# Optimization experiments

Measured on AMD Instinct MI355X. Metric: run time of the kernel, lower is better.

The kernel has to match this reference:

```python
import jax, jax.numpy as jnp
import numpy as np


def setup_inputs() -> dict:
    key = jax.random.key(0)
    ks = jax.random.split(key, 7)
    B, T, D, H, L, NS = 8192, 64, 64, 256, 64, 64  # batch, time, state, hidden, latent, n_shifts
    K = D + L  # Koopman state dim = 128
    x = jax.random.normal(ks[0], (B, T, D), dtype=jnp.float32)
    # Encoder weights stored as [in, out] (math-equivalent to torch Linear).
    W0 = jax.random.normal(ks[1], (D, H), dtype=jnp.float32) / np.float32(np.sqrt(D))
    b0 = jnp.zeros((H,), dtype=jnp.float32)
    W1 = jax.random.normal(ks[2], (H, H), dtype=jnp.float32) / np.float32(np.sqrt(H))
    b1 = jnp.zeros((H,), dtype=jnp.float32)
    W2 = jax.random.normal(ks[3], (H, L), dtype=jnp.float32) / np.float32(np.sqrt(H))  # last layer: no bias
    # Koopman operator scaled so spectral norm ~< 1 (stable 63-step rollout).
    ko_W = jax.random.normal(ks[4], (K, K), dtype=jnp.float32) * np.float32(0.04)
    return {"x": x, "W0": W0, "b0": b0, "W1": W1, "b1": b1, "W2": W2,
            "ko_W": ko_W, "n_shifts": NS}


def reference(x, W0, b0, W1, b1, W2, ko_W, n_shifts):
    x = x[:, :n_shifts, :]                       # [B, NS, D]
    h = jax.nn.relu(x @ W0 + b0)                 # [B, NS, H]
    h = jax.nn.relu(h @ W1 + b1)                 # [B, NS, H]
    z = h @ W2                                   # [B, NS, L] (last layer: no ReLU, no bias)
    enc_gt = jnp.concatenate([x, z], axis=-1)    # [B, NS, D+L]
    z0 = enc_gt[:, 0, :]                         # [B, K]
    def step(c, _):
        nc = c @ ko_W                            # repeated application of ko
        return nc, nc
    _, traj = jax.lax.scan(step, z0, None, length=n_shifts - 1)  # [NS-1, B, K]
    enc_traj = jnp.concatenate([z0[:, None, :], jnp.moveaxis(traj, 0, 1)], axis=1)  # [B, NS, K]
    return enc_gt, enc_traj
```

## Files before the change

kernel.cpp:

```cpp
#include <hip/hip_runtime.h>


typedef __attribute__((ext_vector_type(8))) short short8;
typedef __attribute__((ext_vector_type(4))) float floatx4;

#define DEV __device__ __forceinline__

DEV short f2bf(float f) {
  unsigned u = __builtin_bit_cast(unsigned, f);
  unsigned r = u + 0x7fffu + ((u >> 16) & 1u);
  return (short)(r >> 16);
}

DEV floatx4 zero4() { return (floatx4){0.f, 0.f, 0.f, 0.f}; }

constexpr long ROWS     = 524288;
constexpr long GT_ELEMS = 67108864;
constexpr int  HS_STRIDE = 264;

__global__ void prep_kernel(const float* __restrict__ W0, const float* __restrict__ W1,
                            const float* __restrict__ W2, const float* __restrict__ koW,
                            float* __restrict__ Ppow, short* __restrict__ Wf0,
                            short* __restrict__ Wf1, short* __restrict__ Wf2) {
  int g = blockIdx.x * 256 + threadIdx.x;
  if (g < 2048) {
    int lane = g & 63; int ntkt = g >> 6;
    int n  = ((ntkt >> 1) << 4) + (lane & 15);
    int k0 = (ntkt & 1) * 32 + (lane >> 4) * 8;
    short8 v;
    #pragma unroll
    for (int j = 0; j < 8; ++j) v[j] = f2bf(W0[(k0 + j) * 256 + n]);
    *(short8*)(Wf0 + g * 8) = v;
  } else if (g < 10240) {
    int h = g - 2048;
    int lane = h & 63; int ntkt = h >> 6;
    int n  = ((ntkt >> 3) << 4) + (lane & 15);
    int k0 = (ntkt & 7) * 32 + (lane >> 4) * 8;
    short8 v;
    #pragma unroll
    for (int j = 0; j < 8; ++j) v[j] = f2bf(W1[(k0 + j) * 256 + n]);
    *(short8*)(Wf1 + h * 8) = v;
  } else if (g < 12288) {
    int h = g - 10240;
    int lane = h & 63; int ntkt = h >> 6;
    int n  = ((ntkt >> 3) << 4) + (lane & 15);
    int k0 = (ntkt & 7) * 32 + (lane >> 4) * 8;
    short8 v;
    #pragma unroll
    for (int j = 0; j < 8; ++j) v[j] = f2bf(W2[(k0 + j) * 64 + n]);
    *(short8*)(Wf2 + h * 8) = v;
  } else if (g < 12288 + 8192) {
    int h = g - 12288;
    if (h < 4096) {
      int e = h * 4; int row = e >> 7; int c = e & 127;
      float4 v;
      v.x = (c     == row) ? 1.f : 0.f;
      v.y = (c + 1 == row) ? 1.f : 0.f;
      v.z = (c + 2 == row) ? 1.f : 0.f;
      v.w = (c + 3 == row) ? 1.f : 0.f;
      ((float4*)Ppow)[h] = v;
    } else {
      ((float4*)(Ppow + 16384))[h - 4096] = ((const float4*)koW)[h - 4096];
    }
  }
}

__global__ __launch_bounds__(256) void pow_step(float* Ppow, int base) {
  __shared__ float Bs[128 * 128];
  const int tid = threadIdx.x;
  const int j  = (blockIdx.x >> 2) + 1;
  const int qt = blockIdx.x & 3;
  const float* Bm = Ppow + (long)base * 16384;
  #pragma unroll
  for (int i = 0; i < 16; ++i) {
    int f4 = tid + 256 * i;
    ((float4*)Bs)[f4] = ((const float4*)Bm)[f4];
  }
  __syncthreads();
  const int row = qt * 32 + (tid >> 3);
  const int cg  = (tid & 7) * 16;
  const float* Arow = Ppow + (long)j * 16384 + row * 128;
  float acc[16];
  #pragma unroll
  for (int c = 0; c < 16; ++c) acc[c] = 0.f;
  for (int kk = 0; kk < 128; kk += 4) {
    float4 a4 = *(const float4*)(Arow + kk);
    #pragma unroll
    for (int u = 0; u < 4; ++u) {
      float a = (u == 0) ? a4.x : (u == 1) ? a4.y : (u == 2) ? a4.z : a4.w;
      const float* brow = Bs + (kk + u) * 128 + cg;
      #pragma unroll
      for (int c = 0; c < 16; ++c) acc[c] = fmaf(a, brow[c], acc[c]);
    }
  }
  float* Out = Ppow + (long)(base + j) * 16384 + row * 128 + cg;
  #pragma unroll
  for (int c4 = 0; c4 < 4; ++c4) {
    float4 o; o.x = acc[c4*4]; o.y = acc[c4*4+1]; o.z = acc[c4*4+2]; o.w = acc[c4*4+3];
    *(float4*)(Out + c4 * 4) = o;
  }
}

__global__ void convP_kernel(const float* __restrict__ Ppow, short* __restrict__ Pf) {
  int g = blockIdx.x * 256 + threadIdx.x;
  int lane = g & 63;
  int kt   = (g >> 6) & 3;
  int nt   = g >> 8;
  int n  = nt * 16 + (lane & 15);
  int t  = n >> 7, c = n & 127;
  int k0 = kt * 32 + (lane >> 4) * 8;
  short8 v;
  #pragma unroll
  for (int j = 0; j < 8; ++j) v[j] = f2bf(Ppow[(long)t * 16384 + (k0 + j) * 128 + c]);
  *(short8*)(Pf + (long)g * 8) = v;
}

__global__ __launch_bounds__(256) void mlp_kernel(const float* __restrict__ x,
    const short* __restrict__ Wf0, const float* __restrict__ b0,
    const short* __restrict__ Wf1, const float* __restrict__ b1,
    const short* __restrict__ Wf2, float* __restrict__ out) {
  __shared__ short Hs[64 * HS_STRIDE];
  const int tid  = threadIdx.x;
  const int lane = tid & 63;
  const int wave = tid >> 6;
  const int l15  = lane & 15;
  const int q    = lane >> 4;
  const long rowBase = (long)blockIdx.x * 64;

  #pragma unroll
  for (int i = 0; i < 4; ++i) {
    int f4 = tid + 256 * i;
    int r = f4 >> 4, c4 = f4 & 15;
    float4 v = ((const float4*)(x + (rowBase + r) * 64))[c4];
    ((float4*)(out + (rowBase + r) * 128))[c4] = v;
  }

  floatx4 acc[16];
  #pragma unroll
  for (int nt = 0; nt < 16; ++nt) acc[nt] = zero4();

  #pragma unroll
  for (int kt = 0; kt < 2; ++kt) {
    const float* ap = x + (rowBase + wave * 16 + l15) * 64 + kt * 32 + q * 8;
    float4 a0 = ((const float4*)ap)[0];
    float4 a1 = ((const float4*)ap)[1];
    short8 af;
    af[0]=f2bf(a0.x); af[1]=f2bf(a0.y); af[2]=f2bf(a0.z); af[3]=f2bf(a0.w);
    af[4]=f2bf(a1.x); af[5]=f2bf(a1.y); af[6]=f2bf(a1.z); af[7]=f2bf(a1.w);
    #pragma unroll
    for (int nt = 0; nt < 16; ++nt) {
      short8 bf = *(const short8*)(Wf0 + ((nt * 2 + kt) * 64 + lane) * 8);
      acc[nt] = __builtin_amdgcn_mfma_f32_16x16x32_bf16(af, bf, acc[nt], 0, 0, 0);
    }
  }
  #pragma unroll
  for (int nt = 0; nt < 16; ++nt) {
    int col = nt * 16 + l15;
    float bias = b0[col];
    #pragma unroll
    for (int r = 0; r < 4; ++r) {
      float v = acc[nt][r] + bias;
      Hs[(wave * 16 + q * 4 + r) * HS_STRIDE + col] = f2bf(v > 0.f ? v : 0.f);
    }
    acc[nt] = zero4();
  }
  __syncthreads();

  #pragma unroll
  for (int kt = 0; kt < 8; ++kt) {
    short8 af = *(const short8*)(Hs + (wave * 16 + l15) * HS_STRIDE + kt * 32 + q * 8);
    #pragma unroll
    for (int nt = 0; nt < 16; ++nt) {
      short8 bf = *(const short8*)(Wf1 + ((nt * 8 + kt) * 64 + lane) * 8);
      acc[nt] = __builtin_amdgcn_mfma_f32_16x16x32_bf16(af, bf, acc[nt], 0, 0, 0);
    }
  }
  __syncthreads();
  #pragma unroll
  for (int nt = 0; nt < 16; ++nt) {
    int col = nt * 16 + l15;
    float bias = b1[col];
    #pragma unroll
    for (int r = 0; r < 4; ++r) {
      float v = acc[nt][r] + bias;
      Hs[(wave * 16 + q * 4 + r) * HS_STRIDE + col] = f2bf(v > 0.f ? v : 0.f);
    }
  }
  __syncthreads();

  floatx4 acc2[4];
  #pragma unroll
  for (int nt = 0; nt < 4; ++nt) acc2[nt] = zero4();
  #pragma unroll
  for (int kt = 0; kt < 8; ++kt) {
    short8 af = *(const short8*)(Hs + (wave * 16 + l15) * HS_STRIDE + kt * 32 + q * 8);
    #pragma unroll
    for (int nt = 0; nt < 4; ++nt) {
      short8 bf = *(const short8*)(Wf2 + ((nt * 8 + kt) * 64 + lane) * 8);
      acc2[nt] = __builtin_amdgcn_mfma_f32_16x16x32_bf16(af, bf, acc2[nt], 0, 0, 0);
    }
  }
  #pragma unroll
  for (int nt = 0; nt < 4; ++nt) {
    int col = nt * 16 + l15;
    #pragma unroll
    for (int r = 0; r < 4; ++r)
      out[(rowBase + wave * 16 + q * 4 + r) * 128 + 64 + col] = acc2[nt][r];
  }
}

__global__ __launch_bounds__(256) void traj_kernel(const float* __restrict__ enc_gt,
    const short* __restrict__ Pf, float* __restrict__ out) {
  const int tid  = threadIdx.x;
  const int lane = tid & 63;
  const int wave = tid >> 6;
  const int l15  = lane & 15;
  const int q    = lane >> 4;
  const int bb = blockIdx.x >> 5;
  const int nb = blockIdx.x & 31;
  const long rowBase = (long)bb * 64 + wave * 16;
  const int ntBase = nb * 16;

  floatx4 acc[16];
  #pragma unroll
  for (int nt = 0; nt < 16; ++nt) acc[nt] = zero4();

  #pragma unroll
  for (int kt = 0; kt < 4; ++kt) {
    const float* ap = enc_gt + (rowBase + l15) * 8192 + kt * 32 + q * 8;
    float4 a0 = ((const float4*)ap)[0];
    float4 a1 = ((const float4*)ap)[1];
    short8 af;
    af[0]=f2bf(a0.x); af[1]=f2bf(a0.y); af[2]=f2bf(a0.z); af[3]=f2bf(a0.w);
    af[4]=f2bf(a1.x); af[5]=f2bf(a1.y); af[6]=f2bf(a1.z); af[7]=f2bf(a1.w);
    #pragma unroll
    for (int nt = 0; nt < 16; ++nt) {
      short8 bf = *(const short8*)(Pf + (((long)(ntBase + nt) * 4 + kt) * 64 + lane) * 8);
      acc[nt] = __builtin_amdgcn_mfma_f32_16x16x32_bf16(af, bf, acc[nt], 0, 0, 0);
    }
  }
  #pragma unroll
  for (int nt = 0; nt < 16; ++nt) {
    long col = (long)(ntBase + nt) * 16 + l15;
    #pragma unroll
    for (int r = 0; r < 4; ++r)
      out[GT_ELEMS + (rowBase + q * 4 + r) * 8192 + col] = acc[nt][r];
  }
}

extern "C" void kernel_launch(void* const* d_in, const int* in_sizes, int n_in,
                              void* d_out, int out_size, void* d_ws, size_t ws_size,
                              hipStream_t stream) {
  (void)in_sizes; (void)n_in; (void)out_size; (void)ws_size;
  const float* x   = (const float*)d_in[0];
  const float* W0  = (const float*)d_in[1];
  const float* b0  = (const float*)d_in[2];
  const float* W1  = (const float*)d_in[3];
  const float* b1  = (const float*)d_in[4];
  const float* W2  = (const float*)d_in[5];
  const float* koW = (const float*)d_in[6];
  float* out = (float*)d_out;

  char* ws = (char*)d_ws;
  float* Ppow = (float*)ws;
  short* Pf   = (short*)(ws + 4194304);
  short* Wf0  = (short*)(ws + 6291456);
  short* Wf1  = (short*)(ws + 6324224);
  short* Wf2  = (short*)(ws + 6455296);

  hipLaunchKernelGGL(prep_kernel, dim3(80), dim3(256), 0, stream,
                     W0, W1, W2, koW, Ppow, Wf0, Wf1, Wf2);
  const int bases[6] = {1, 2, 4, 8, 16, 32};
  const int cnts[6]  = {1, 2, 4, 8, 16, 31};
  for (int s = 0; s < 6; ++s)
    hipLaunchKernelGGL(pow_step, dim3(cnts[s] * 4), dim3(256), 0, stream, Ppow, bases[s]);
  hipLaunchKernelGGL(convP_kernel, dim3(512), dim3(256), 0, stream, Ppow, Pf);
  hipLaunchKernelGGL(mlp_kernel, dim3(8192), dim3(256), 0, stream,
                     x, Wf0, b0, Wf1, b1, Wf2, out);
  hipLaunchKernelGGL(traj_kernel, dim3(4096), dim3(256), 0, stream, out, Pf, out);
}
```

Before: 1.120 ms.

## Split MFMA tiles across waves by N and stage A-tile in LDS

In both the MLP and trajectory kernels, each wave now owns a 4-column-tile slice of the output for all 64 rows, where before it owned 16 rows across every column tile. Each wave therefore loads only 4 B fragments per k-step instead of 16, which cuts redundant global weight and Pf reads across waves. The trajectory kernel also converts the block's 64x128 enc_gt tile to bf16 once into shared memory, replacing per-wave global loads and conversions. Launch bounds add a minimum of 4 blocks per CU, which caps register use and may cause spills. The kernel is dominated by the large trajectory output write, so the gain may be limited.

```diff
diff --git a/kernel.cpp b/kernel.cpp
--- a/kernel.cpp
+++ b/kernel.cpp
@@ -2,6 +2,7 @@
 
 
 typedef __attribute__((ext_vector_type(8))) short short8;
+typedef __attribute__((ext_vector_type(4))) short sshort4;
 typedef __attribute__((ext_vector_type(4))) float floatx4;
 
 #define DEV __device__ __forceinline__
@@ -17,6 +18,7 @@
 constexpr long ROWS     = 524288;
 constexpr long GT_ELEMS = 67108864;
 constexpr int  HS_STRIDE = 264;
+constexpr int  AS_STRIDE = 136;
 
 __global__ void prep_kernel(const float* __restrict__ W0, const float* __restrict__ W1,
                             const float* __restrict__ W2, const float* __restrict__ koW,
@@ -115,7 +117,7 @@
   *(short8*)(Pf + (long)g * 8) = v;
 }
 
-__global__ __launch_bounds__(256) void mlp_kernel(const float* __restrict__ x,
+__global__ __launch_bounds__(256, 4) void mlp_kernel(const float* __restrict__ x,
     const short* __restrict__ Wf0, const float* __restrict__ b0,
     const short* __restrict__ Wf1, const float* __restrict__ b1,
     const short* __restrict__ Wf2, float* __restrict__ out) {
@@ -125,6 +127,7 @@
   const int wave = tid >> 6;
   const int l15  = lane & 15;
   const int q    = lane >> 4;
+  const int ntg  = wave * 4;
   const long rowBase = (long)blockIdx.x * 64;
 
   #pragma unroll
@@ -135,82 +138,100 @@
     ((float4*)(out + (rowBase + r) * 128))[c4] = v;
   }
 
-  floatx4 acc[16];
-  #pragma unroll
-  for (int nt = 0; nt < 16; ++nt) acc[nt] = zero4();
+  floatx4 acc[4][4];
+  #pragma unroll
+  for (int m = 0; m < 4; ++m)
+    #pragma unroll
+    for (int nt = 0; nt < 4; ++nt) acc[m][nt] = zero4();
 
   #pragma unroll
   for (int kt = 0; kt < 2; ++kt) {
-    const float* ap = x + (rowBase + wave * 16 + l15) * 64 + kt * 32 + q * 8;
-    float4 a0 = ((const float4*)ap)[0];
-    float4 a1 = ((const float4*)ap)[1];
-    short8 af;
-    af[0]=f2bf(a0.x); af[1]=f2bf(a0.y); af[2]=f2bf(a0.z); af[3]=f2bf(a0.w);
-    af[4]=f2bf(a1.x); af[5]=f2bf(a1.y); af[6]=f2bf(a1.z); af[7]=f2bf(a1.w);
-    #pragma unroll
-    for (int nt = 0; nt < 16; ++nt) {
-      short8 bf = *(const short8*)(Wf0 + ((nt * 2 + kt) * 64 + lane) * 8);
-      acc[nt] = __builtin_amdgcn_mfma_f32_16x16x32_bf16(af, bf, acc[nt], 0, 0, 0);
-    }
-  }
-  #pragma unroll
-  for (int nt = 0; nt < 16; ++nt) {
-    int col = nt * 16 + l15;
+    short8 bfr[4];
+    #pragma unroll
+    for (int nt = 0; nt < 4; ++nt)
+      bfr[nt] = *(const short8*)(Wf0 + (((ntg + nt) * 2 + kt) * 64 + lane) * 8);
+    #pragma unroll
+    for (int m = 0; m < 4; ++m) {
+      const float* ap = x + (rowBase + m * 16 + l15) * 64 + kt * 32 + q * 8;
+      float4 a0 = ((const float4*)ap)[0];
+      float4 a1 = ((const float4*)ap)[1];
+      short8 af;
+      af[0]=f2bf(a0.x); af[1]=f2bf(a0.y); af[2]=f2bf(a0.z); af[3]=f2bf(a0.w);
+      af[4]=f2bf(a1.x); af[5]=f2bf(a1.y); af[6]=f2bf(a1.z); af[7]=f2bf(a1.w);
+      #pragma unroll
+      for (int nt = 0; nt < 4; ++nt)
+        acc[m][nt] = __builtin_amdgcn_mfma_f32_16x16x32_bf16(af, bfr[nt], acc[m][nt], 0, 0, 0);
+    }
+  }
+  #pragma unroll
+  for (int nt = 0; nt < 4; ++nt) {
+    int col = (ntg + nt) * 16 + l15;
     float bias = b0[col];
     #pragma unroll
-    for (int r = 0; r < 4; ++r) {
-      float v = acc[nt][r] + bias;
-      Hs[(wave * 16 + q * 4 + r) * HS_STRIDE + col] = f2bf(v > 0.f ? v : 0.f);
-    }
-    acc[nt] = zero4();
+    for (int m = 0; m < 4; ++m) {
+      #pragma unroll
+      for (int r = 0; r < 4; ++r) {
+        float v = acc[m][nt][r] + bias;
+        Hs[(m * 16 + q * 4 + r) * HS_STRIDE + col] = f2bf(v > 0.f ? v : 0.f);
+      }
+      acc[m][nt] = zero4();
+    }
   }
   __syncthreads();
 
   #pragma unroll
   for (int kt = 0; kt < 8; ++kt) {
-    short8 af = *(const short8*)(Hs + (wave * 16 + l15) * HS_STRIDE + kt * 32 + q * 8);
-    #pragma unroll
-    for (int nt = 0; nt < 16; ++nt) {
-      short8 bf = *(const short8*)(Wf1 + ((nt * 8 + kt) * 64 + lane) * 8);
-      acc[nt] = __builtin_amdgcn_mfma_f32_16x16x32_bf16(af, bf, acc[nt], 0, 0, 0);
-    }
-  }
-  __syncthreads();
-  #pragma unroll
-  for (int nt = 0; nt < 16; ++nt) {
-    int col = nt * 16 + l15;
+    short8 bfr[4];
+    #pragma unroll
+    for (int nt = 0; nt < 4; ++nt)
+      bfr[nt] = *(const short8*)(Wf1 + (((ntg + nt) * 8 + kt) * 64 + lane) * 8);
+    #pragma unroll
+    for (int m = 0; m < 4; ++m) {
+      short8 af = *(const short8*)(Hs + (m * 16 + l15) * HS_STRIDE + kt * 32 + q * 8);
+      #pragma unroll
+      for (int nt = 0; nt < 4; ++nt)
+        acc[m][nt] = __builtin_amdgcn_mfma_f32_16x16x32_bf16(af, bfr[nt], acc[m][nt], 0, 0, 0);
+    }
+  }
+  __syncthreads();
+  #pragma unroll
+  for (int nt = 0; nt < 4; ++nt) {
+    int col = (ntg + nt) * 16 + l15;
     float bias = b1[col];
     #pragma unroll
-    for (int r = 0; r < 4; ++r) {
-      float v = acc[nt][r] + bias;
-      Hs[(wave * 16 + q * 4 + r) * HS_STRIDE + col] = f2bf(v > 0.f ? v : 0.f);
+    for (int m = 0; m < 4; ++m) {
+      #pragma unroll
+      for (int r = 0; r < 4; ++r) {
+        float v = acc[m][nt][r] + bias;
+        Hs[(m * 16 + q * 4 + r) * HS_STRIDE + col] = f2bf(v > 0.f ? v : 0.f);
+      }
     }
   }
   __syncthreads();
 
   floatx4 acc2[4];
   #pragma unroll
-  for (int nt = 0; nt < 4; ++nt) acc2[nt] = zero4();
+  for (int m = 0; m < 4; ++m) acc2[m] = zero4();
   #pragma unroll
   for (int kt = 0; kt < 8; ++kt) {
-    short8 af = *(const short8*)(Hs + (wave * 16 + l15) * HS_STRIDE + kt * 32 + q * 8);
-    #pragma unroll
-    for (int nt = 0; nt < 4; ++nt) {
-      short8 bf = *(const short8*)(Wf2 + ((nt * 8 + kt) * 64 + lane) * 8);
-      acc2[nt] = __builtin_amdgcn_mfma_f32_16x16x32_bf16(af, bf, acc2[nt], 0, 0, 0);
-    }
-  }
-  #pragma unroll
-  for (int nt = 0; nt < 4; ++nt) {
-    int col = nt * 16 + l15;
+    short8 bfr = *(const short8*)(Wf2 + ((wave * 8 + kt) * 64 + lane) * 8);
+    #pragma unroll
+    for (int m = 0; m < 4; ++m) {
+      short8 af = *(const short8*)(Hs + (m * 16 + l15) * HS_STRIDE + kt * 32 + q * 8);
+      acc2[m] = __builtin_amdgcn_mfma_f32_16x16x32_bf16(af, bfr, acc2[m], 0, 0, 0);
+    }
+  }
+  #pragma unroll
+  for (int m = 0; m < 4; ++m) {
     #pragma unroll
     for (int r = 0; r < 4; ++r)
-      out[(rowBase + wave * 16 + q * 4 + r) * 128 + 64 + col] = acc2[nt][r];
-  }
-}
-
-__global__ __launch_bounds__(256) void traj_kernel(const float* __restrict__ enc_gt,
+      out[(rowBase + m * 16 + q * 4 + r) * 128 + 64 + wave * 16 + l15] = acc2[m][r];
+  }
+}
+
+__global__ __launch_bounds__(256, 4) void traj_kernel(const float* __restrict__ enc_gt,
     const short* __restrict__ Pf, float* __restrict__ out) {
+  __shared__ short As[64 * AS_STRIDE];
   const int tid  = threadIdx.x;
   const int lane = tid & 63;
   const int wave = tid >> 6;
@@ -218,33 +239,49 @@
   const int q    = lane >> 4;
   const int bb = blockIdx.x >> 5;
   const int nb = blockIdx.x & 31;
-  const long rowBase = (long)bb * 64 + wave * 16;
-  const int ntBase = nb * 16;
-
-  floatx4 acc[16];
-  #pragma unroll
-  for (int nt = 0; nt < 16; ++nt) acc[nt] = zero4();
+  const long rowBase = (long)bb * 64;
+  const int ntg = nb * 16 + wave * 4;
+
+  #pragma unroll
+  for (int i = 0; i < 8; ++i) {
+    int idx = tid + 256 * i;
+    int r = idx >> 5, c4 = idx & 31;
+    float4 v = ((const float4*)(enc_gt + (rowBase + r) * 8192))[c4];
+    sshort4 s;
+    s[0] = f2bf(v.x); s[1] = f2bf(v.y); s[2] = f2bf(v.z); s[3] = f2bf(v.w);
+    *(sshort4*)(As + r * AS_STRIDE + c4 * 4) = s;
+  }
+  __syncthreads();
+
+  floatx4 acc[4][4];
+  #pragma unroll
+  for (int m = 0; m < 4; ++m)
+    #pragma unroll
+    for (int nt = 0; nt < 4; ++nt) acc[m][nt] = zero4();
 
   #pragma unroll
   for (int kt = 0; kt < 4; ++kt) {
-    const float* ap = enc_gt + (rowBase + l15) * 8192 + kt * 32 + q * 8;
-    float4 a0 = ((const float4*)ap)[0];
-    float4 a1 = ((const float4*)ap)[1];
-    short8 af;
-    af[0]=f2bf(a0.x); af[1]=f2bf(a0.y); af[2]=f2bf(a0.z); af[3]=f2bf(a0.w);
-    af[4]=f2bf(a1.x); af[5]=f2bf(a1.y); af[6]=f2bf(a1.z); af[7]=f2bf(a1.w);
-    #pragma unroll
-    for (int nt = 0; nt < 16; ++nt) {
-      short8 bf = *(const short8*)(Pf + (((long)(ntBase + nt) * 4 + kt) * 64 + lane) * 8);
-      acc[nt] = __builtin_amdgcn_mfma_f32_16x16x32_bf16(af, bf, acc[nt], 0, 0, 0);
-    }
-  }
-  #pragma unroll
-  for (int nt = 0; nt < 16; ++nt) {
-    long col = (long)(ntBase + nt) * 16 + l15;
-    #pragma unroll
-    for (int r = 0; r < 4; ++r)
-      out[GT_ELEMS + (rowBase + q * 4 + r) * 8192 + col] = acc[nt][r];
+    short8 bfr[4];
+    #pragma unroll
+    for (int nt = 0; nt < 4; ++nt)
+      bfr[nt] = *(const short8*)(Pf + (((long)(ntg + nt) * 4 + kt) * 64 + lane) * 8);
+    #pragma unroll
+    for (int m = 0; m < 4; ++m) {
+      short8 af = *(const short8*)(As + (m * 16 + l15) * AS_STRIDE + kt * 32 + q * 8);
+      #pragma unroll
+      for (int nt = 0; nt < 4; ++nt)
+        acc[m][nt] = __builtin_amdgcn_mfma_f32_16x16x32_bf16(af, bfr[nt], acc[m][nt], 0, 0, 0);
+    }
+  }
+  #pragma unroll
+  for (int m = 0; m < 4; ++m) {
+    #pragma unroll
+    for (int nt = 0; nt < 4; ++nt) {
+      long col = (long)(ntg + nt) * 16 + l15;
+      #pragma unroll
+      for (int r = 0; r < 4; ++r)
+        out[GT_ELEMS + (rowBase + m * 16 + q * 4 + r) * 8192 + col] = acc[m][nt][r];
+    }
   }
 }
 
```

Result: faster. 1.012 ms (-9.7%).
